# Optimization experiments

Measured on AMD Instinct MI355X. Metric: run time of the kernel, lower is better.

## Reference

```python
import jax, jax.numpy as jnp
import numpy as np

V = 10000      # num graph nodes
DEG = 32       # avg degree
B = 16         # batch
K = 6          # Chebyshev order
EPS = 1e-5


def _bn(x, g, b):
    # training-mode BatchNorm1d; x is (B,C,V) or (B,C)
    ax = (0, 2) if x.ndim == 3 else (0,)
    m = jnp.mean(x, axis=ax, keepdims=True)
    v = jnp.var(x, axis=ax, keepdims=True)
    shp = (1, -1, 1) if x.ndim == 3 else (1, -1)
    return (x - m) * jax.lax.rsqrt(v + EPS) * g.reshape(shp) + b.reshape(shp)


def _cheb(lap_idx, lap_vals, x, w, bias=None):
    # x: (B,Cin,V); w: (K,Cin,Cout); sparse laplacian as COO (row,col,val)
    b, cin, v = x.shape
    k = w.shape[0]
    row, col = lap_idx[0], lap_idx[1]

    def spmm(z):  # z: (V, Cin*B)
        return jax.ops.segment_sum(lap_vals[:, None] * z[col], row, num_segments=V)

    x0 = jnp.transpose(x, (2, 1, 0)).reshape(v, cin * b)
    xs = [x0]
    if k > 1:
        x1 = spmm(x0)
        xs.append(x1)
        for _ in range(2, k):
            x2 = 2.0 * spmm(x1) - x0
            xs.append(x2)
            x0, x1 = x1, x2
    xk = jnp.stack(xs).reshape(k, v, cin, b)
    out = jnp.einsum('kvcb,kco->bov', xk, w)  # (B,Cout,V)
    if bias is not None:
        out = out + bias[None, :, None]
    return out


def _block(lap_idx, lap_vals, h, g_in, b_in, w_a, ba, g_h, b_h, w_b, bb, sc_w):
    xb = _bn(h, g_in, b_in)
    o = _cheb(lap_idx, lap_vals, xb, w_a, ba)
    o = jax.nn.relu(o)
    o = _bn(o, g_h, b_h)
    o = _cheb(lap_idx, lap_vals, o, w_b, bb)
    short = _cheb(lap_idx, lap_vals, xb, sc_w, None)  # K=1 shortcut, no bias
    return jax.nn.relu(o + short)


def setup_inputs() -> dict:
    rng = np.random.default_rng(0)
    # graph edges: each node has DEG random neighbors
    row = np.repeat(np.arange(V), DEG)
    col = rng.integers(0, V, size=V * DEG)
    w = rng.random(V * DEG).astype(np.float32) + 0.1
    deg = np.zeros(V, np.float32)
    np.add.at(deg, row, w)
    deg = np.maximum(deg, 1e-6)
    # rescaled laplacian with lmax=2: 2L/lmax - I = -D^-1/2 W D^-1/2
    vals = (-w / np.sqrt(deg[row] * deg[col])).astype(np.float32)
    lap_idx = jnp.asarray(np.stack([row, col]).astype(np.int32))
    lap_vals = jnp.asarray(vals)

    key = jax.random.key(0)
    ks = iter(jax.random.split(key, 32))
    n = lambda *s: jax.random.normal(next(ks), s, jnp.float32) * 0.05
    return {
        'x': jax.random.normal(next(ks), (B, 8, V), jnp.float32),
        'w_in': n(K, 8, 32), 'b_in': jnp.zeros((32,), jnp.float32),
        'g1': jnp.ones((32,), jnp.float32), 'be1': jnp.zeros((32,), jnp.float32),
        'w1a': n(K, 32, 64), 'b1a': jnp.zeros((64,), jnp.float32),
        'g1h': jnp.ones((64,), jnp.float32), 'be1h': jnp.zeros((64,), jnp.float32),
        'w1b': n(K, 64, 64), 'b1b': jnp.zeros((64,), jnp.float32),
        'sc1': n(1, 32, 64),
        'g2': jnp.ones((64,), jnp.float32), 'be2': jnp.zeros((64,), jnp.float32),
        'w2a': n(K, 64, 128), 'b2a': jnp.zeros((128,), jnp.float32),
        'g2h': jnp.ones((128,), jnp.float32), 'be2h': jnp.zeros((128,), jnp.float32),
        'w2b': n(K, 128, 128), 'b2b': jnp.zeros((128,), jnp.float32),
        'sc2': n(1, 64, 128),
        'g_out': jnp.ones((128,), jnp.float32), 'be_out': jnp.zeros((128,), jnp.float32),
        'lin_w': n(128, 10), 'lin_b': jnp.zeros((10,), jnp.float32),
        'lap_vals': lap_vals, 'lap_idx': lap_idx,
    }


def reference(x, w_in, b_in, g1, be1, w1a, b1a, g1h, be1h, w1b, b1b, sc1,
              g2, be2, w2a, b2a, g2h, be2h, w2b, b2b, sc2,
              g_out, be_out, lin_w, lin_b, lap_vals, lap_idx):
    out = jax.nn.relu(_cheb(lap_idx, lap_vals, x, w_in, b_in))
    out = _block(lap_idx, lap_vals, out, g1, be1, w1a, b1a, g1h, be1h, w1b, b1b, sc1)
    out = _block(lap_idx, lap_vals, out, g2, be2, w2a, b2a, g2h, be2h, w2b, b2b, sc2)
    out = jnp.max(out, axis=2)            # global max pool over nodes -> (B,C)
    out = _bn(out, g_out, be_out)
    out = jax.nn.relu(out @ lin_w + lin_b)
    return jax.nn.log_softmax(out, axis=1)
```

## Files before the change

kernel.cpp:

```cpp
#include <hip/hip_runtime.h>
#include <hip/hip_bf16.h>

#define V 10000
#define DEG 32
#define NNZ (V * DEG)
#define EPS 1e-5f
#define TPV 384

typedef __hip_bfloat16 bf16;
typedef _Float16 f16;
typedef unsigned short ushort16;
typedef f16 half8 __attribute__((ext_vector_type(8)));
typedef __attribute__((ext_vector_type(4))) float f32x4;

__device__ __forceinline__ float b2f(bf16 v) { return __bfloat162float(v); }
__device__ __forceinline__ float ldin(const void* p, size_t i, int isb) {
    return isb ? b2f(((const bf16*)p)[i]) : ((const float*)p)[i];
}

__global__ void k_probe(const unsigned* __restrict__ g1, int* __restrict__ flag) {
    if (threadIdx.x == 0 && blockIdx.x == 0)
        *flag = (g1[0] == 0x3F803F80u) ? 1 : 0;
}

__global__ void k_edgeprep(unsigned* __restrict__ ep, const int* __restrict__ col,
                           const void* __restrict__ vals, const int* __restrict__ dflag) {
    int i = blockIdx.x * 256 + threadIdx.x;
    if (i >= NNZ) return;
    union { f16 h; ushort16 u; } q;
    q.h = (f16)ldin(vals, i, *dflag);
    ep[i] = (unsigned)col[i] | ((unsigned)q.u << 16);
}

__global__ void k_transpose(const void* __restrict__ x, f16* __restrict__ trm,
                            const int* __restrict__ dflag) {
    const int isb = *dflag;
    __shared__ float tile[128 * 33];
    int v0 = blockIdx.x * 32;
    int tid = threadIdx.x;
    for (int i = tid; i < 128 * 32; i += 256) {
        int cbi = i >> 5, vi = i & 31;
        int v = v0 + vi;
        tile[cbi * 33 + vi] = (v < V) ? ldin(x, (size_t)cbi * V + v, isb) : 0.f;
    }
    __syncthreads();
    for (int i = tid; i < 32 * 128; i += 256) {
        int vi = i >> 7, cbo = i & 127;
        int c = cbo >> 4, b = cbo & 15;
        int v = v0 + vi;
        if (v < V)
            trm[((size_t)v * 16 + b) * TPV + c] = (f16)tile[(b * 8 + c) * 33 + vi];
    }
}

__global__ void k_wprep(f16* __restrict__ wt, const void* __restrict__ w,
                        int Cin, int Cout, int WTP, int GW, int span,
                        const int* __restrict__ dflag) {
    const int isb = *dflag;
    int i = blockIdx.x * 256 + threadIdx.x;
    if (i >= Cout * span) return;
    int o = i / span, q = i - o * span;
    int fill = q / (6 * GW), qq = q - fill * (6 * GW);
    int j = qq / GW, gc = qq - j * GW;
    int c = fill * GW + gc;
    float val = 0.f;
    if (j < 6 && c < Cin) val = ldin(w, ((size_t)j * Cin + c) * Cout + o, isb);
    wt[(size_t)o * WTP + q] = (f16)val;
}

__global__ void k_wscprep(f16* __restrict__ wsc, const void* __restrict__ w,
                          int Cin, int Cout, const int* __restrict__ dflag) {
    const int isb = *dflag;
    int i = blockIdx.x * 256 + threadIdx.x;
    if (i >= Cout * Cin) return;
    int o = i / Cin, c = i - o * Cin;
    wsc[i] = (f16)ldin(w, (size_t)c * Cout + o, isb);
}

__global__ __launch_bounds__(256) void k_spmm6(
        f16* __restrict__ trm, const unsigned* __restrict__ ep, int L,
        int kZ, int kP, int kW, float alpha, float beta) {
    extern __shared__ char smem[];
    int lanes = 2 * L;
    int NPB = 256 / lanes;
    int* ec = (int*)smem;
    float* ev = (float*)(ec + NPB * 32);
    int blk = blockIdx.x;
    int sub = blk & 7;
    int vg = blk >> 3;
    int tid = threadIdx.x;
    for (int i = tid; i < NPB * 32; i += 256) {
        size_t e = (size_t)vg * (NPB * 32) + i;
        unsigned p = (e < NNZ) ? ep[e] : 0u;
        ec[i] = (int)(p & 0xFFFFu);
        union { ushort16 u; f16 h; } q; q.u = (ushort16)(p >> 16);
        ev[i] = (float)q.h;
    }
    __syncthreads();
    int n = tid / lanes;
    int r = tid - n * lanes;
    int b = sub * 2 + (r >= L ? 1 : 0);
    int l = (r >= L) ? r - L : r;
    int v = vg * NPB + n;
    if (v >= V) return;
    const int* ecn = ec + n * 32;
    const float* evn = ev + n * 32;
    int lofs = l * 8;
    float acc[8];
#pragma unroll
    for (int i = 0; i < 8; ++i) acc[i] = 0.f;
#pragma unroll 4
    for (int jj = 0; jj < 32; ++jj) {
        int u = ecn[jj];
        float f = evn[jj];
        half8 zz = *(const half8*)(trm + ((size_t)u * 16 + b) * TPV + kZ + lofs);
#pragma unroll
        for (int i = 0; i < 8; ++i) acc[i] += f * (float)zz[i];
    }
    size_t rowv = ((size_t)v * 16 + b) * TPV + lofs;
    half8 out;
    if (kP >= 0) {
        half8 pv = __builtin_nontemporal_load((const half8*)(trm + rowv + kP));
#pragma unroll
        for (int i = 0; i < 8; ++i)
            out[i] = (f16)(alpha * acc[i] + beta * (float)pv[i]);
    } else {
#pragma unroll
        for (int i = 0; i < 8; ++i) out[i] = (f16)(alpha * acc[i]);
    }
    __builtin_nontemporal_store(out, (half8*)(trm + rowv + kW));
}

template <int M16, int KS, int NW>
__global__ __launch_bounds__(NW * 64) void k_gemm9(
        f16* __restrict__ C, const f16* __restrict__ trm,
        const f16* __restrict__ wt, int WTP, int wtBase,
        const void* __restrict__ bias,
        const f16* __restrict__ xb, const f16* __restrict__ wsc, int Ksc,
        int relu, const int* __restrict__ dflag) {
    extern __shared__ f16 aw[];
    constexpr int Cout = M16 * 16;
    constexpr int KCH = (KS == 12) ? 4 : KS;
    constexpr int kchunks = KS / KCH;
    constexpr int pitch = KCH * 32 + 8;
    int tid = threadIdx.x;
    int wave = tid >> 6, lane = tid & 63;
    int v = blockIdx.x * NW + wave;
    int bcol = lane & 15, kq = lane >> 4;

    const f16* brow = trm + ((size_t)v * 16 + bcol) * TPV + kq * 8;
    half8 breg[KS];
#pragma unroll
    for (int ks = 0; ks < KS; ++ks) breg[ks] = *(const half8*)(brow + ks * 32);
    half8 xreg0, xreg1;
    if (Ksc > 0) {
        const f16* xrow = xb + ((size_t)v * 16 + bcol) * Ksc + kq * 8;
        xreg0 = *(const half8*)xrow;
        if (Ksc > 32) xreg1 = *(const half8*)(xrow + 32);
    }

    f32x4 acc[M16];
    if (bias) {
        const int isb = *dflag;
#pragma unroll
        for (int mt = 0; mt < M16; ++mt) {
            int ob = mt * 16 + kq * 4;
#pragma unroll
            for (int r = 0; r < 4; ++r) acc[mt][r] = ldin(bias, ob + r, isb);
        }
    } else {
#pragma unroll
        for (int mt = 0; mt < M16; ++mt) {
            int ob = mt * 16 + kq * 4;
#pragma unroll
            for (int r = 0; r < 4; ++r)
                acc[mt][r] = (float)C[(size_t)v * (Cout * 16) + (ob + r) * 16 + bcol];
        }
    }

#pragma unroll
    for (int kc = 0; kc < kchunks; ++kc) {
        int kcb = kc * KCH * 32;
        int total = Cout * KCH * 32;
        for (int idx = tid * 8; idx < total; idx += NW * 64 * 8) {
            int o = idx / (KCH * 32), q = idx - o * (KCH * 32);
            half8 w8 = *(const half8*)(wt + (size_t)o * WTP + wtBase + kcb + q);
            *(half8*)&aw[o * pitch + q] = w8;
        }
        __syncthreads();
#pragma unroll
        for (int ks = 0; ks < KCH; ++ks) {
            half8 bf = breg[kc * KCH + ks];
#pragma unroll
            for (int mt = 0; mt < M16; ++mt) {
                half8 af = *(const half8*)&aw[(mt * 16 + bcol) * pitch + ks * 32 + kq * 8];
                acc[mt] = __builtin_amdgcn_mfma_f32_16x16x32_f16(af, bf, acc[mt], 0, 0, 0);
            }
        }
        __syncthreads();
    }

    if (Ksc > 0) {
#pragma unroll
        for (int mt = 0; mt < M16; ++mt) {
            const f16* ap = wsc + (size_t)(mt * 16 + bcol) * Ksc + kq * 8;
            half8 af = *(const half8*)ap;
            acc[mt] = __builtin_amdgcn_mfma_f32_16x16x32_f16(af, xreg0, acc[mt], 0, 0, 0);
        }
        if (Ksc > 32) {
#pragma unroll
            for (int mt = 0; mt < M16; ++mt) {
                const f16* ap = wsc + (size_t)(mt * 16 + bcol) * Ksc + 32 + kq * 8;
                half8 af = *(const half8*)ap;
                acc[mt] = __builtin_amdgcn_mfma_f32_16x16x32_f16(af, xreg1, acc[mt], 0, 0, 0);
            }
        }
    }

#pragma unroll
    for (int mt = 0; mt < M16; ++mt) {
        int ob = mt * 16 + kq * 4;
#pragma unroll
        for (int r = 0; r < 4; ++r) {
            float val = acc[mt][r];
            if (relu) val = fmaxf(val, 0.f);
            C[(size_t)v * (Cout * 16) + (ob + r) * 16 + bcol] = (f16)val;
        }
    }
}

__global__ void k_bnzero(float* __restrict__ s) { s[threadIdx.x] = 0.f; }

__global__ void k_bnpart(const f16* __restrict__ H, int C,
                         float* __restrict__ s1, float* __restrict__ s2) {
    int c = blockIdx.x, part = blockIdx.y, tid = threadIdx.x;
    int W = C * 16;
    int v0 = part * 400;
    float a1 = 0.f, a2 = 0.f;
    for (int i = tid; i < 400 * 16; i += 256) {
        float x = (float)H[(size_t)(v0 + (i >> 4)) * W + c * 16 + (i & 15)];
        a1 += x; a2 += x * x;
    }
    __shared__ float r1[4], r2[4];
    for (int off = 32; off > 0; off >>= 1) {
        a1 += __shfl_down(a1, off);
        a2 += __shfl_down(a2, off);
    }
    int wv = tid >> 6;
    if ((tid & 63) == 0) { r1[wv] = a1; r2[wv] = a2; }
    __syncthreads();
    if (tid == 0) {
        atomicAdd(&s1[c], r1[0] + r1[1] + r1[2] + r1[3]);
        atomicAdd(&s2[c], r2[0] + r2[1] + r2[2] + r2[3]);
    }
}

__global__ void k_bnfinal(const float* __restrict__ s1, const float* __restrict__ s2,
                          int C, float* __restrict__ mean, float* __restrict__ rstd) {
    int c = threadIdx.x;
    if (c >= C) return;
    const float inv = 1.f / (float)(V * 16);
    float m = s1[c] * inv;
    float var = s2[c] * inv - m * m;
    mean[c] = m;
    rstd[c] = rsqrtf(var + EPS);
}

__global__ void k_bnapply(const f16* __restrict__ H, int C, int total,
                          const float* __restrict__ mean, const float* __restrict__ rstd,
                          const void* __restrict__ g, const void* __restrict__ be,
                          f16* __restrict__ trm, int trmC,
                          f16* __restrict__ xb, int xbOff, int xbC,
                          const int* __restrict__ dflag) {
    const int isb = *dflag;
    int i = blockIdx.x * 256 + threadIdx.x;
    if (i >= total) return;
    int W = C * 16;
    int v = i / W, rem = i - v * W;
    int c = rem >> 4, b = rem & 15;
    float val = ((float)H[i] - mean[c]) * rstd[c] * ldin(g, c, isb) + ldin(be, c, isb);
    if (c < trmC)
        trm[((size_t)v * 16 + b) * TPV + c] = (f16)val;
    if (xb && c >= xbOff)
        xb[((size_t)v * 16 + b) * xbC + (c - xbOff)] = (f16)val;
}

__global__ void k_seedhi(f16* __restrict__ trm, const f16* __restrict__ xb) {
    int i = blockIdx.x * 256 + threadIdx.x;
    if (i >= V * 16 * 64) return;
    int row = i >> 6, c = i & 63;
    trm[(size_t)row * TPV + c] = xb[i];
}

__global__ void k_pool_init(unsigned* P) { P[blockIdx.x * 256 + threadIdx.x] = 0u; }

__global__ void k_pool(const f16* __restrict__ H, unsigned* __restrict__ P) {
    int t = blockIdx.x * 256 + threadIdx.x;
    int v0 = blockIdx.y * 250;
    float m = 0.f;
    for (int v = v0; v < v0 + 250; ++v) m = fmaxf(m, (float)H[(size_t)v * 2048 + t]);
    atomicMax(&P[t], __float_as_uint(m));
}

__global__ void k_head(const float* __restrict__ Pf, const void* __restrict__ g,
                       const void* __restrict__ be, const void* __restrict__ lw,
                       const void* __restrict__ lb, float* __restrict__ out,
                       const int* __restrict__ dflag) {
    const int isb = *dflag;
    __shared__ float pn[128 * 17];
    __shared__ float logits[160];
    __shared__ float mx[16], se[16];
    int tid = threadIdx.x;
    if (tid < 128) {
        int c = tid;
        float s1 = 0.f, s2 = 0.f;
        for (int b = 0; b < 16; ++b) {
            float x = Pf[c * 16 + b];
            s1 += x; s2 += x * x;
        }
        float m = s1 * (1.f / 16.f);
        float var = s2 * (1.f / 16.f) - m * m;
        float rs = rsqrtf(var + EPS);
        float gg = ldin(g, c, isb), bb = ldin(be, c, isb);
        for (int b = 0; b < 16; ++b)
            pn[c * 17 + b] = (Pf[c * 16 + b] - m) * rs * gg + bb;
    }
    __syncthreads();
    if (tid < 160) {
        int b = tid / 10, o = tid % 10;
        float a = ldin(lb, o, isb);
        for (int c = 0; c < 128; ++c) a += pn[c * 17 + b] * ldin(lw, c * 10 + o, isb);
        logits[tid] = fmaxf(a, 0.f);
    }
    __syncthreads();
    if (tid < 16) {
        float m = -1e30f;
        for (int o = 0; o < 10; ++o) m = fmaxf(m, logits[tid * 10 + o]);
        float s = 0.f;
        for (int o = 0; o < 10; ++o) s += expf(logits[tid * 10 + o] - m);
        mx[tid] = m;
        se[tid] = logf(s);
    }
    __syncthreads();
    if (tid < 160) {
        int b = tid / 10;
        out[tid] = logits[tid] - mx[b] - se[b];
    }
}

static void run_bn(const f16* H, int C, float* s1, float* s2, float* mean,
                   float* rstd, f16* trm, int trmC, f16* xb, int xbOff, int xbC,
                   const void* g, const void* be, const int* dflag, hipStream_t s) {
    int total = V * C * 16;
    k_bnzero<<<1, 512, 0, s>>>(s1);
    k_bnpart<<<dim3(C, 25), 256, 0, s>>>(H, C, s1, s2);
    k_bnfinal<<<1, 128, 0, s>>>(s1, s2, C, mean, rstd);
    k_bnapply<<<(total + 255) / 256, 256, 0, s>>>(H, C, total, mean, rstd, g, be,
                                                  trm, trmC, xb, xbOff, xbC, dflag);
}

static void run_group(f16* trm, const unsigned* ep, int L, int GW, hipStream_t s) {
    int lanes = 2 * L, NPB = 256 / lanes;
    dim3 g(((V + NPB - 1) / NPB) * 8), blk(256);
    size_t lds = (size_t)NPB * 32 * 8;
    k_spmm6<<<g, blk, lds, s>>>(trm, ep, L, 0 * GW, -1,     1 * GW, 1.f,  0.f);
    k_spmm6<<<g, blk, lds, s>>>(trm, ep, L, 1 * GW, 0 * GW, 2 * GW, 2.f, -1.f);
    k_spmm6<<<g, blk, lds, s>>>(trm, ep, L, 2 * GW, 1 * GW, 3 * GW, 2.f, -1.f);
    k_spmm6<<<g, blk, lds, s>>>(trm, ep, L, 3 * GW, 2 * GW, 4 * GW, 2.f, -1.f);
    k_spmm6<<<g, blk, lds, s>>>(trm, ep, L, 4 * GW, 3 * GW, 5 * GW, 2.f, -1.f);
}

template <int M16, int KS, int NW>
static void launch_g9(f16* C, const f16* trm, const f16* wt, int WTP, int wtBase,
                      const void* bias, const f16* xb, const f16* wsc, int Ksc,
                      int relu, const int* dflag, hipStream_t s) {
    constexpr int KCH = (KS == 12) ? 4 : KS;
    size_t lds = (size_t)(M16 * 16) * (KCH * 32 + 8) * sizeof(f16);
    k_gemm9<M16, KS, NW><<<V / NW, NW * 64, lds, s>>>(C, trm, wt, WTP, wtBase,
                                                      bias, xb, wsc, Ksc, relu, dflag);
}

extern "C" void kernel_launch(void* const* d_in, const int* in_sizes, int n_in,
                              void* d_out, int out_size, void* d_ws, size_t ws_size,
                              hipStream_t stream) {
    (void)in_sizes; (void)n_in; (void)out_size; (void)ws_size;
    const void* x      = d_in[0];
    const void* w_in   = d_in[1];
    const void* b_in   = d_in[2];
    const void* g1     = d_in[3];
    const void* be1    = d_in[4];
    const void* w1a    = d_in[5];
    const void* b1a    = d_in[6];
    const void* g1h    = d_in[7];
    const void* be1h   = d_in[8];
    const void* w1b    = d_in[9];
    const void* b1b    = d_in[10];
    const void* sc1    = d_in[11];
    const void* g2     = d_in[12];
    const void* be2    = d_in[13];
    const void* w2a    = d_in[14];
    const void* b2a    = d_in[15];
    const void* g2h    = d_in[16];
    const void* be2h   = d_in[17];
    const void* w2b    = d_in[18];
    const void* b2b    = d_in[19];
    const void* sc2    = d_in[20];
    const void* g_out  = d_in[21];
    const void* be_out = d_in[22];
    const void* lin_w  = d_in[23];
    const void* lin_b  = d_in[24];
    const void* lap_vals = d_in[25];
    const int*  lap_idx  = (const int*)d_in[26];
    const int* col = lap_idx + NNZ;

    float* ws = (float*)d_ws;
    f16* Cbuf = (f16*)ws;
    f16* TRM  = (f16*)(ws + (size_t)10240000);
    f16* XBT1 = (f16*)(ws + (size_t)40960000);
    f16* XBT2 = (f16*)(ws + (size_t)43520000);
    f16* XBH  = (f16*)(ws + (size_t)48640000);
    f16* WT   = (f16*)(ws + (size_t)53760000);
    f16* WSC  = WT + 128 * 768;
    float* s1p = (float*)(WSC + 128 * 64);
    float* s2p = s1p + 256;
    float* meanp = s2p + 256;
    float* rstdp = meanp + 128;
    unsigned* P = (unsigned*)(rstdp + 128);
    unsigned* EP = P + 2048;
    int* dflag = (int*)(EP + NNZ);

    k_probe<<<1, 64, 0, stream>>>((const unsigned*)g1, dflag);
    k_edgeprep<<<(NNZ + 255) / 256, 256, 0, stream>>>(EP, col, lap_vals, dflag);

    k_transpose<<<(V + 31) / 32, 256, 0, stream>>>(x, TRM, dflag);
    k_wprep<<<(32 * 64 + 255) / 256, 256, 0, stream>>>(WT, w_in, 8, 32, 64, 8, 64, dflag);
    run_group(TRM, EP, 1, 8, stream);
    f16* H1 = Cbuf;
    launch_g9<2, 2, 4>(H1, TRM, WT, 64, 0, b_in, nullptr, nullptr, 0, 1, dflag, stream);

    run_bn(H1, 32, s1p, s2p, meanp, rstdp, TRM, 32, XBT1, 0, 32, g1, be1, dflag, stream);
    k_wprep<<<(64 * 192 + 255) / 256, 256, 0, stream>>>(WT, w1a, 32, 64, 192, 32, 192, dflag);
    run_group(TRM, EP, 4, 32, stream);
    f16* ACCa1 = Cbuf;
    launch_g9<4, 6, 4>(ACCa1, TRM, WT, 192, 0, b1a, nullptr, nullptr, 0, 1, dflag, stream);

    run_bn(ACCa1, 64, s1p, s2p, meanp, rstdp, TRM, 64, nullptr, 0, 0, g1h, be1h, dflag, stream);
    k_wprep<<<(64 * 384 + 255) / 256, 256, 0, stream>>>(WT, w1b, 64, 64, 384, 64, 384, dflag);
    run_group(TRM, EP, 8, 64, stream);
    k_wscprep<<<(64 * 32 + 255) / 256, 256, 0, stream>>>(WSC, sc1, 32, 64, dflag);
    f16* ACCb1 = Cbuf;
    launch_g9<4, 12, 8>(ACCb1, TRM, WT, 384, 0, b1b, XBT1, WSC, 32, 1, dflag, stream);
    f16* H2 = ACCb1;

    run_bn(H2, 64, s1p, s2p, meanp, rstdp, TRM, 64, XBT2, 0, 64, g2, be2, dflag, stream);
    k_wprep<<<(128 * 384 + 255) / 256, 256, 0, stream>>>(WT, w2a, 64, 128, 384, 64, 384, dflag);
    run_group(TRM, EP, 8, 64, stream);
    f16* ACCa2 = Cbuf;
    launch_g9<8, 12, 8>(ACCa2, TRM, WT, 384, 0, b2a, nullptr, nullptr, 0, 1, dflag, stream);

    run_bn(ACCa2, 128, s1p, s2p, meanp, rstdp, TRM, 64, XBH, 64, 64, g2h, be2h, dflag, stream);
    k_wprep<<<(128 * 768 + 255) / 256, 256, 0, stream>>>(WT, w2b, 128, 128, 768, 64, 768, dflag);
    run_group(TRM, EP, 8, 64, stream);
    k_wscprep<<<(128 * 64 + 255) / 256, 256, 0, stream>>>(WSC, sc2, 64, 128, dflag);
    f16* ACCb2 = Cbuf;
    launch_g9<8, 12, 8>(ACCb2, TRM, WT, 768, 0, b2b, XBT2, WSC, 64, 0, dflag, stream);
    k_seedhi<<<(V * 16 * 64 + 255) / 256, 256, 0, stream>>>(TRM, XBH);
    run_group(TRM, EP, 8, 64, stream);
    launch_g9<8, 12, 8>(ACCb2, TRM, WT, 768, 384, nullptr, nullptr, nullptr, 0, 1, dflag, stream);

    k_pool_init<<<8, 256, 0, stream>>>(P);
    k_pool<<<dim3(8, 40), 256, 0, stream>>>(ACCb2, P);
    k_head<<<1, 256, 0, stream>>>((const float*)P, g_out, be_out, lin_w, lin_b,
                                  (float*)d_out, dflag);
}
```

Before: 1.871 ms.

## Fuse BN statistics and max-pool into GEMM epilogues, batch weight prep

The GEMM epilogue now reduces per-channel sum and sum of squares with wave shuffles and LDS, then adds them atomically to global BN statistics. This removes the separate zero, partial-reduce and finalize kernels, and bnapply now computes mean and rstd on the fly. The final GEMM does the global max-pool in its epilogue instead of writing the activation and re-reading it. All weight and shortcut prep is merged into one launch at the start. The cost is extra atomics and LDS traffic in the GEMM epilogue, plus float atomic ordering nondeterminism.

```diff
diff --git a/kernel.cpp b/kernel.cpp
--- a/kernel.cpp
+++ b/kernel.cpp
@@ -21,6 +21,12 @@
 __global__ void k_probe(const unsigned* __restrict__ g1, int* __restrict__ flag) {
     if (threadIdx.x == 0 && blockIdx.x == 0)
         *flag = (g1[0] == 0x3F803F80u) ? 1 : 0;
+}
+
+__global__ void k_zeroall(float* __restrict__ stats, unsigned* __restrict__ P) {
+    int t = threadIdx.x;
+    for (int i = t; i < 2048; i += 256) stats[i] = 0.f;
+    for (int i = t; i < 2048; i += 256) P[i] = 0u;
 }
 
 __global__ void k_edgeprep(unsigned* __restrict__ ep, const int* __restrict__ col,
@@ -53,28 +59,35 @@
     }
 }
 
-__global__ void k_wprep(f16* __restrict__ wt, const void* __restrict__ w,
-                        int Cin, int Cout, int WTP, int GW, int span,
-                        const int* __restrict__ dflag) {
+__global__ void k_wprep_all(f16* __restrict__ wt,
+                            const void* w_in, const void* w1a, const void* w1b,
+                            const void* w2a, const void* w2b,
+                            const void* sc1, const void* sc2,
+                            const int* __restrict__ dflag) {
     const int isb = *dflag;
     int i = blockIdx.x * 256 + threadIdx.x;
-    if (i >= Cout * span) return;
-    int o = i / span, q = i - o * span;
-    int fill = q / (6 * GW), qq = q - fill * (6 * GW);
-    int j = qq / GW, gc = qq - j * GW;
-    int c = fill * GW + gc;
-    float val = 0.f;
-    if (j < 6 && c < Cin) val = ldin(w, ((size_t)j * Cin + c) * Cout + o, isb);
-    wt[(size_t)o * WTP + q] = (f16)val;
-}
-
-__global__ void k_wscprep(f16* __restrict__ wsc, const void* __restrict__ w,
-                          int Cin, int Cout, const int* __restrict__ dflag) {
-    const int isb = *dflag;
-    int i = blockIdx.x * 256 + threadIdx.x;
-    if (i >= Cout * Cin) return;
-    int o = i / Cin, c = i - o * Cin;
-    wsc[i] = (f16)ldin(w, (size_t)c * Cout + o, isb);
+    if (i >= 196608) return;
+    const void* w; int Cin, Cout, span, GW, base; int isSC = 0;
+    if (i < 2048)        { w = w_in; Cin = 8;   Cout = 32;  span = 64;  GW = 8;  base = 0; }
+    else if (i < 14336)  { w = w1a;  Cin = 32;  Cout = 64;  span = 192; GW = 32; base = 2048; }
+    else if (i < 38912)  { w = w1b;  Cin = 64;  Cout = 64;  span = 384; GW = 64; base = 14336; }
+    else if (i < 88064)  { w = w2a;  Cin = 64;  Cout = 128; span = 384; GW = 64; base = 38912; }
+    else if (i < 186368) { w = w2b;  Cin = 128; Cout = 128; span = 768; GW = 64; base = 88064; }
+    else if (i < 188416) { w = sc1;  Cin = 32;  Cout = 64;  span = 32;  GW = 0;  base = 186368; isSC = 1; }
+    else                 { w = sc2;  Cin = 64;  Cout = 128; span = 64;  GW = 0;  base = 188416; isSC = 1; }
+    int e = i - base;
+    int o = e / span, q = e - o * span;
+    float val;
+    if (isSC) {
+        val = ldin(w, (size_t)q * Cout + o, isb);
+    } else {
+        int fill = q / (6 * GW), qq = q - fill * (6 * GW);
+        int j = qq / GW, gc = qq - j * GW;
+        int c = fill * GW + gc;
+        val = 0.f;
+        if (j < 6 && c < Cin) val = ldin(w, ((size_t)j * Cin + c) * Cout + o, isb);
+    }
+    wt[i] = (f16)val;
 }
 
 __global__ __launch_bounds__(256) void k_spmm6(
@@ -131,13 +144,14 @@
     __builtin_nontemporal_store(out, (half8*)(trm + rowv + kW));
 }
 
-template <int M16, int KS, int NW>
-__global__ __launch_bounds__(NW * 64) void k_gemm9(
+template <int M16, int KS, int NW, int EPI>
+__global__ __launch_bounds__(NW * 64) void k_gemm10(
         f16* __restrict__ C, const f16* __restrict__ trm,
         const f16* __restrict__ wt, int WTP, int wtBase,
         const void* __restrict__ bias,
         const f16* __restrict__ xb, const f16* __restrict__ wsc, int Ksc,
-        int relu, const int* __restrict__ dflag) {
+        int relu, float* __restrict__ gs1, float* __restrict__ gs2,
+        unsigned* __restrict__ Pg, const int* __restrict__ dflag) {
     extern __shared__ f16 aw[];
     constexpr int Cout = M16 * 16;
     constexpr int KCH = (KS == 12) ? 4 : KS;
@@ -224,61 +238,87 @@
         for (int r = 0; r < 4; ++r) {
             float val = acc[mt][r];
             if (relu) val = fmaxf(val, 0.f);
-            C[(size_t)v * (Cout * 16) + (ob + r) * 16 + bcol] = (f16)val;
-        }
-    }
-}
-
-__global__ void k_bnzero(float* __restrict__ s) { s[threadIdx.x] = 0.f; }
-
-__global__ void k_bnpart(const f16* __restrict__ H, int C,
-                         float* __restrict__ s1, float* __restrict__ s2) {
-    int c = blockIdx.x, part = blockIdx.y, tid = threadIdx.x;
-    int W = C * 16;
-    int v0 = part * 400;
-    float a1 = 0.f, a2 = 0.f;
-    for (int i = tid; i < 400 * 16; i += 256) {
-        float x = (float)H[(size_t)(v0 + (i >> 4)) * W + c * 16 + (i & 15)];
-        a1 += x; a2 += x * x;
-    }
-    __shared__ float r1[4], r2[4];
-    for (int off = 32; off > 0; off >>= 1) {
-        a1 += __shfl_down(a1, off);
-        a2 += __shfl_down(a2, off);
-    }
-    int wv = tid >> 6;
-    if ((tid & 63) == 0) { r1[wv] = a1; r2[wv] = a2; }
-    __syncthreads();
-    if (tid == 0) {
-        atomicAdd(&s1[c], r1[0] + r1[1] + r1[2] + r1[3]);
-        atomicAdd(&s2[c], r2[0] + r2[1] + r2[2] + r2[3]);
-    }
-}
-
-__global__ void k_bnfinal(const float* __restrict__ s1, const float* __restrict__ s2,
-                          int C, float* __restrict__ mean, float* __restrict__ rstd) {
-    int c = threadIdx.x;
-    if (c >= C) return;
-    const float inv = 1.f / (float)(V * 16);
-    float m = s1[c] * inv;
-    float var = s2[c] * inv - m * m;
-    mean[c] = m;
-    rstd[c] = rsqrtf(var + EPS);
+            acc[mt][r] = val;
+            if (EPI != 2)
+                C[(size_t)v * (Cout * 16) + (ob + r) * 16 + bcol] = (f16)val;
+        }
+    }
+
+    if (EPI == 1) {
+        float* ls1 = (float*)aw;
+        float* ls2 = ls1 + NW * Cout;
+#pragma unroll
+        for (int mt = 0; mt < M16; ++mt) {
+#pragma unroll
+            for (int r = 0; r < 4; ++r) {
+                float a = acc[mt][r];
+                float b2 = a * a;
+#pragma unroll
+                for (int m = 1; m < 16; m <<= 1) {
+                    a += __shfl_xor(a, m);
+                    b2 += __shfl_xor(b2, m);
+                }
+                if (bcol == 0) {
+                    int ch = mt * 16 + kq * 4 + r;
+                    ls1[wave * Cout + ch] = a;
+                    ls2[wave * Cout + ch] = b2;
+                }
+            }
+        }
+        __syncthreads();
+        for (int i = tid; i < Cout; i += NW * 64) {
+            float t1 = 0.f, t2 = 0.f;
+#pragma unroll
+            for (int w = 0; w < NW; ++w) {
+                t1 += ls1[w * Cout + i];
+                t2 += ls2[w * Cout + i];
+            }
+            atomicAdd(&gs1[i], t1);
+            atomicAdd(&gs2[i], t2);
+        }
+    } else if (EPI == 2) {
+        unsigned* lp = (unsigned*)aw;
+        for (int i = tid; i < Cout * 16; i += NW * 64) lp[i] = 0u;
+        __syncthreads();
+#pragma unroll
+        for (int mt = 0; mt < M16; ++mt) {
+            int ob = mt * 16 + kq * 4;
+#pragma unroll
+            for (int r = 0; r < 4; ++r)
+                atomicMax(&lp[(ob + r) * 16 + bcol], __float_as_uint(acc[mt][r]));
+        }
+        __syncthreads();
+        for (int i = tid; i < Cout * 16; i += NW * 64)
+            atomicMax(&Pg[i], lp[i]);
+    }
 }
 
 __global__ void k_bnapply(const f16* __restrict__ H, int C, int total,
-                          const float* __restrict__ mean, const float* __restrict__ rstd,
+                          const float* __restrict__ s1, const float* __restrict__ s2,
                           const void* __restrict__ g, const void* __restrict__ be,
                           f16* __restrict__ trm, int trmC,
                           f16* __restrict__ xb, int xbOff, int xbC,
                           const int* __restrict__ dflag) {
+    __shared__ float lm[16], lr[16];
     const int isb = *dflag;
-    int i = blockIdx.x * 256 + threadIdx.x;
+    int W = C * 16;
+    int base = blockIdx.x * 256;
+    int cbase = (base % W) >> 4;
+    if (threadIdx.x < 16) {
+        int c = cbase + threadIdx.x;
+        const float inv = 1.f / (float)(V * 16);
+        float m = s1[c] * inv;
+        float var = s2[c] * inv - m * m;
+        lm[threadIdx.x] = m;
+        lr[threadIdx.x] = rsqrtf(var + EPS);
+    }
+    __syncthreads();
+    int i = base + threadIdx.x;
     if (i >= total) return;
-    int W = C * 16;
     int v = i / W, rem = i - v * W;
     int c = rem >> 4, b = rem & 15;
-    float val = ((float)H[i] - mean[c]) * rstd[c] * ldin(g, c, isb) + ldin(be, c, isb);
+    float val = ((float)H[i] - lm[c - cbase]) * lr[c - cbase] * ldin(g, c, isb)
+                + ldin(be, c, isb);
     if (c < trmC)
         trm[((size_t)v * 16 + b) * TPV + c] = (f16)val;
     if (xb && c >= xbOff)
@@ -290,16 +330,6 @@
     if (i >= V * 16 * 64) return;
     int row = i >> 6, c = i & 63;
     trm[(size_t)row * TPV + c] = xb[i];
-}
-
-__global__ void k_pool_init(unsigned* P) { P[blockIdx.x * 256 + threadIdx.x] = 0u; }
-
-__global__ void k_pool(const f16* __restrict__ H, unsigned* __restrict__ P) {
-    int t = blockIdx.x * 256 + threadIdx.x;
-    int v0 = blockIdx.y * 250;
-    float m = 0.f;
-    for (int v = v0; v < v0 + 250; ++v) m = fmaxf(m, (float)H[(size_t)v * 2048 + t]);
-    atomicMax(&P[t], __float_as_uint(m));
 }
 
 __global__ void k_head(const float* __restrict__ Pf, const void* __restrict__ g,
@@ -348,17 +378,6 @@
     }
 }
 
-static void run_bn(const f16* H, int C, float* s1, float* s2, float* mean,
-                   float* rstd, f16* trm, int trmC, f16* xb, int xbOff, int xbC,
-                   const void* g, const void* be, const int* dflag, hipStream_t s) {
-    int total = V * C * 16;
-    k_bnzero<<<1, 512, 0, s>>>(s1);
-    k_bnpart<<<dim3(C, 25), 256, 0, s>>>(H, C, s1, s2);
-    k_bnfinal<<<1, 128, 0, s>>>(s1, s2, C, mean, rstd);
-    k_bnapply<<<(total + 255) / 256, 256, 0, s>>>(H, C, total, mean, rstd, g, be,
-                                                  trm, trmC, xb, xbOff, xbC, dflag);
-}
-
 static void run_group(f16* trm, const unsigned* ep, int L, int GW, hipStream_t s) {
     int lanes = 2 * L, NPB = 256 / lanes;
     dim3 g(((V + NPB - 1) / NPB) * 8), blk(256);
@@ -370,14 +389,18 @@
     k_spmm6<<<g, blk, lds, s>>>(trm, ep, L, 4 * GW, 3 * GW, 5 * GW, 2.f, -1.f);
 }
 
-template <int M16, int KS, int NW>
-static void launch_g9(f16* C, const f16* trm, const f16* wt, int WTP, int wtBase,
-                      const void* bias, const f16* xb, const f16* wsc, int Ksc,
-                      int relu, const int* dflag, hipStream_t s) {
+template <int M16, int KS, int NW, int EPI>
+static void launch_g10(f16* C, const f16* trm, const f16* wt, int WTP, int wtBase,
+                       const void* bias, const f16* xb, const f16* wsc, int Ksc,
+                       int relu, float* gs1, float* gs2, unsigned* Pg,
+                       const int* dflag, hipStream_t s) {
     constexpr int KCH = (KS == 12) ? 4 : KS;
     size_t lds = (size_t)(M16 * 16) * (KCH * 32 + 8) * sizeof(f16);
-    k_gemm9<M16, KS, NW><<<V / NW, NW * 64, lds, s>>>(C, trm, wt, WTP, wtBase,
-                                                      bias, xb, wsc, Ksc, relu, dflag);
+    size_t need = (EPI == 1) ? (size_t)NW * M16 * 16 * 2 * 4
+                 : (EPI == 2) ? (size_t)M16 * 16 * 16 * 4 : 0;
+    if (need > lds) lds = need;
+    k_gemm10<M16, KS, NW, EPI><<<V / NW, NW * 64, lds, s>>>(
+        C, trm, wt, WTP, wtBase, bias, xb, wsc, Ksc, relu, gs1, gs2, Pg, dflag);
 }
 
 extern "C" void kernel_launch(void* const* d_in, const int* in_sizes, int n_in,
@@ -420,56 +443,68 @@
     f16* XBT2 = (f16*)(ws + (size_t)43520000);
     f16* XBH  = (f16*)(ws + (size_t)48640000);
     f16* WT   = (f16*)(ws + (size_t)53760000);
-    f16* WSC  = WT + 128 * 768;
-    float* s1p = (float*)(WSC + 128 * 64);
-    float* s2p = s1p + 256;
-    float* meanp = s2p + 256;
-    float* rstdp = meanp + 128;
-    unsigned* P = (unsigned*)(rstdp + 128);
+    float* STATS = ws + (size_t)53760000 + 98304;
+    unsigned* P = (unsigned*)(STATS + 2048);
     unsigned* EP = P + 2048;
     int* dflag = (int*)(EP + NNZ);
 
+    f16* WT_L1 = WT;
+    f16* WT_A1 = WT + 2048;
+    f16* WT_B1 = WT + 14336;
+    f16* WT_A2 = WT + 38912;
+    f16* WT_B2 = WT + 88064;
+    f16* WSC1  = WT + 186368;
+    f16* WSC2  = WT + 188416;
+    float* S0 = STATS;
+    float* S1 = STATS + 512;
+    float* S2 = STATS + 1024;
+    float* S3 = STATS + 1536;
+
     k_probe<<<1, 64, 0, stream>>>((const unsigned*)g1, dflag);
+    k_zeroall<<<1, 256, 0, stream>>>(STATS, P);
     k_edgeprep<<<(NNZ + 255) / 256, 256, 0, stream>>>(EP, col, lap_vals, dflag);
+    k_wprep_all<<<(196608 + 255) / 256, 256, 0, stream>>>(
+        WT, w_in, w1a, w1b, w2a, w2b, sc1, sc2, dflag);
 
     k_transpose<<<(V + 31) / 32, 256, 0, stream>>>(x, TRM, dflag);
-    k_wprep<<<(32 * 64 + 255) / 256, 256, 0, stream>>>(WT, w_in, 8, 32, 64, 8, 64, dflag);
     run_group(TRM, EP, 1, 8, stream);
     f16* H1 = Cbuf;
-    launch_g9<2, 2, 4>(H1, TRM, WT, 64, 0, b_in, nullptr, nullptr, 0, 1, dflag, stream);
-
-    run_bn(H1, 32, s1p, s2p, meanp, rstdp, TRM, 32, XBT1, 0, 32, g1, be1, dflag, stream);
-    k_wprep<<<(64 * 192 + 255) / 256, 256, 0, stream>>>(WT, w1a, 32, 64, 192, 32, 192, dflag);
+    launch_g10<2, 2, 4, 1>(H1, TRM, WT_L1, 64, 0, b_in, nullptr, nullptr, 0, 1,
+                           S0, S0 + 256, P, dflag, stream);
+
+    k_bnapply<<<(V * 512) / 256, 256, 0, stream>>>(H1, 32, V * 512, S0, S0 + 256,
+                                                   g1, be1, TRM, 32, XBT1, 0, 32, dflag);
     run_group(TRM, EP, 4, 32, stream);
     f16* ACCa1 = Cbuf;
-    launch_g9<4, 6, 4>(ACCa1, TRM, WT, 192, 0, b1a, nullptr, nullptr, 0, 1, dflag, stream);
-
-    run_bn(ACCa1, 64, s1p, s2p, meanp, rstdp, TRM, 64, nullptr, 0, 0, g1h, be1h, dflag, stream);
-    k_wprep<<<(64 * 384 + 255) / 256, 256, 0, stream>>>(WT, w1b, 64, 64, 384, 64, 384, dflag);
+    launch_g10<4, 6, 4, 1>(ACCa1, TRM, WT_A1, 192, 0, b1a, nullptr, nullptr, 0, 1,
+                           S1, S1 + 256, P, dflag, stream);
+
+    k_bnapply<<<(V * 1024) / 256, 256, 0, stream>>>(ACCa1, 64, V * 1024, S1, S1 + 256,
+                                                    g1h, be1h, TRM, 64, nullptr, 0, 0, dflag);
     run_group(TRM, EP, 8, 64, stream);
-    k_wscprep<<<(64 * 32 + 255) / 256, 256, 0, stream>>>(WSC, sc1, 32, 64, dflag);
     f16* ACCb1 = Cbuf;
-    launch_g9<4, 12, 8>(ACCb1, TRM, WT, 384, 0, b1b, XBT1, WSC, 32, 1, dflag, stream);
+    launch_g10<4, 12, 8, 1>(ACCb1, TRM, WT_B1, 384, 0, b1b, XBT1, WSC1, 32, 1,
+                            S2, S2 + 256, P, dflag, stream);
     f16* H2 = ACCb1;
 
-    run_bn(H2, 64, s1p, s2p, meanp, rstdp, TRM, 64, XBT2, 0, 64, g2, be2, dflag, stream);
-    k_wprep<<<(128 * 384 + 255) / 256, 256, 0, stream>>>(WT, w2a, 64, 128, 384, 64, 384, dflag);
+    k_bnapply<<<(V * 1024) / 256, 256, 0, stream>>>(H2, 64, V * 1024, S2, S2 + 256,
+                                                    g2, be2, TRM, 64, XBT2, 0, 64, dflag);
     run_group(TRM, EP, 8, 64, stream);
     f16* ACCa2 = Cbuf;
-    launch_g9<8, 12, 8>(ACCa2, TRM, WT, 384, 0, b2a, nullptr, nullptr, 0, 1, dflag, stream);
-
-    run_bn(ACCa2, 128, s1p, s2p, meanp, rstdp, TRM, 64, XBH, 64, 64, g2h, be2h, dflag, stream);
-    k_wprep<<<(128 * 768 + 255) / 256, 256, 0, stream>>>(WT, w2b, 128, 128, 768, 64, 768, dflag);
+    launch_g10<8, 12, 8, 1>(ACCa2, TRM, WT_A2, 384, 0, b2a, nullptr, nullptr, 0, 1,
+                            S3, S3 + 256, P, dflag, stream);
+
+    k_bnapply<<<(V * 2048) / 256, 256, 0, stream>>>(ACCa2, 128, V * 2048, S3, S3 + 256,
+                                                    g2h, be2h, TRM, 64, XBH, 64, 64, dflag);
     run_group(TRM, EP, 8, 64, stream);
-    k_wscprep<<<(128 * 64 + 255) / 256, 256, 0, stream>>>(WSC, sc2, 64, 128, dflag);
     f16* ACCb2 = Cbuf;
-    launch_g9<8, 12, 8>(ACCb2, TRM, WT, 768, 0, b2b, XBT2, WSC, 64, 0, dflag, stream);
+    launch_g10<8, 12, 8, 0>(ACCb2, TRM, WT_B2, 768, 0, b2b, XBT2, WSC2, 64, 0,
+                            nullptr, nullptr, P, dflag, stream);
     k_seedhi<<<(V * 16 * 64 + 255) / 256, 256, 0, stream>>>(TRM, XBH);
     run_group(TRM, EP, 8, 64, stream);
-    launch_g9<8, 12, 8>(ACCb2, TRM, WT, 768, 384, nullptr, nullptr, nullptr, 0, 1, dflag, stream);
-
-    k_pool_init<<<8, 256, 0, stream>>>(P);
-    k_pool<<<dim3(8, 40), 256, 0, stream>>>(ACCb2, P);
+    launch_g10<8, 12, 8, 2>(ACCb2, TRM, WT_B2, 768, 384, nullptr, nullptr, nullptr, 0, 1,
+                            nullptr, nullptr, P, dflag, stream);
+
     k_head<<<1, 256, 0, stream>>>((const float*)P, g_out, be_out, lin_w, lin_b,
                                   (float*)d_out, dflag);
 }
```

Measured after the change: 1.900 ms. No clear change (+1.5%).
